# Kernel tuning notes

Measured on AMD Instinct MI355X. Metric: run time of the kernel, lower is better.

## Reference

```python
import jax, jax.numpy as jnp
import numpy as np

E = 1024      # embed_dim (== embed_dim_)
NH = 8        # num_heads
HD = E // NH  # head_dim
BS1 = 2048
BS2 = 2048
EPS = 1e-5


def _layernorm(x, g, b):
    m = jnp.mean(x, axis=-1, keepdims=True)
    v = jnp.mean(jnp.square(x - m), axis=-1, keepdims=True)
    return (x - m) * jax.lax.rsqrt(v + EPS) * g + b


def setup_inputs() -> dict:
    key = jax.random.key(0)
    ks = jax.random.split(key, 16)
    s = 1.0 / np.sqrt(E)
    s4 = 1.0 / np.sqrt(4 * E)
    inp = {
        "x1": jax.random.normal(ks[0], (BS1, E), jnp.float32),
        "x2": jax.random.normal(ks[1], (BS2, E), jnp.float32),
        "Wq": jax.random.uniform(ks[2], (E, E), jnp.float32, -s, s),
        "bq": jax.random.uniform(ks[3], (E,), jnp.float32, -s, s),
        "Wk": jax.random.uniform(ks[4], (E, E), jnp.float32, -s, s),
        "bk": jax.random.uniform(ks[5], (E,), jnp.float32, -s, s),
        "Wv": jax.random.uniform(ks[6], (E, E), jnp.float32, -s, s),
        "bv": jax.random.uniform(ks[7], (E,), jnp.float32, -s, s),
        "Wo": jax.random.uniform(ks[8], (E, E), jnp.float32, -s, s),
        "bo": jax.random.uniform(ks[9], (E,), jnp.float32, -s, s),
        "W1": jax.random.uniform(ks[10], (4 * E, E), jnp.float32, -s, s),
        "b1": jax.random.uniform(ks[11], (4 * E,), jnp.float32, -s, s),
        "W2": jax.random.uniform(ks[12], (E, 4 * E), jnp.float32, -s4, s4),
        "b2": jax.random.uniform(ks[13], (E,), jnp.float32, -s4, s4),
        "g1": jnp.ones((E,), jnp.float32),
        "be1": jnp.zeros((E,), jnp.float32),
        "g2": jnp.ones((E,), jnp.float32),
        "be2": jnp.zeros((E,), jnp.float32),
    }
    return inp


def reference(x1, x2, Wq, bq, Wk, bk, Wv, bv, Wo, bo, W1, b1, W2, b2, g1, be1, g2, be2):
    scale = HD ** -0.5
    # Projections; attention runs over the batch axis (n=bs1, m=bs2)
    q = (x1 @ Wq.T + bq).reshape(BS1, NH, HD)   # [n,h,d]
    k = (x2 @ Wk.T + bk).reshape(BS2, NH, HD)   # [m,h,d]
    v = (x2 @ Wv.T + bv).reshape(BS2, NH, HD)   # [m,h,d]
    scores = jnp.einsum('nhd,mhd->nmh', q, k) * scale  # [n,m,h]
    # NOTE: faithful to source: softmax over the HEADS axis (dim=-1)
    probs = jax.nn.softmax(scores, axis=-1)
    # dropout is identity in eval mode
    attn = jnp.einsum('nmh,mhd->nhd', probs, v).reshape(BS1, E)
    attn = attn @ Wo.T + bo
    h = _layernorm(x1 + attn, g1, be1)
    ffn = jax.nn.relu(h @ W1.T + b1) @ W2.T + b2
    return _layernorm(h + ffn, g2, be2)
```

## Files before the change

kernel.cpp:

```cpp
#include <hip/hip_runtime.h>

#define BS 2048
#define EMB 1024
#define NHEAD 8
#define HDIM 128

typedef unsigned short u16;
typedef __attribute__((ext_vector_type(8))) short bf16x8;
typedef __attribute__((ext_vector_type(4))) float f32x4;

__device__ __forceinline__ u16 f32_bf16(float f) {
  unsigned u = __float_as_uint(f);
  u += 0x7fffu + ((u >> 16) & 1u);
  return (u16)(u >> 16);
}
__device__ __forceinline__ float bf2f(u16 x) {
  return __uint_as_float((unsigned)x << 16);
}

__device__ __forceinline__ void gld_lds16(const void* g, void* l) {
  __builtin_amdgcn_global_load_lds(
      (const __attribute__((address_space(1))) void*)g,
      (__attribute__((address_space(3))) void*)l, 16, 0, 0);
}

struct CvtArgs { const float* src[8]; };
__global__ __launch_bounds__(256) void cvt_all(CvtArgs a, u16* __restrict__ dst) {
  long i = (long)blockIdx.x * 256 + threadIdx.x;
  int seg = (int)(i >> 18);
  const float* src; long b;
  if (seg < 2)       { src = a.src[0]; b = 0; }
  else if (seg < 4)  { src = a.src[1]; b = 2L << 18; }
  else if (seg == 4) { src = a.src[2]; b = 4L << 18; }
  else if (seg == 5) { src = a.src[3]; b = 5L << 18; }
  else if (seg == 6) { src = a.src[4]; b = 6L << 18; }
  else if (seg == 7) { src = a.src[5]; b = 7L << 18; }
  else if (seg < 12) { src = a.src[6]; b = 8L << 18; }
  else               { src = a.src[7]; b = 12L << 18; }
  float4 v = ((const float4*)src)[i - b];
  ushort4 o;
  o.x = f32_bf16(v.x); o.y = f32_bf16(v.y); o.z = f32_bf16(v.z); o.w = f32_bf16(v.w);
  ((ushort4*)dst)[i] = o;
}

__device__ __forceinline__ void gemm_core(
    const u16* __restrict__ A, const u16* __restrict__ B, void* __restrict__ Cp,
    const float* __restrict__ bias, int K, int lda, int ldb, int ldc,
    long cbase, int mode, int relu, int m0, int n0) {
  __shared__ __align__(16) u16 As[128 * 32];
  __shared__ __align__(16) u16 Bs[128 * 32];
  const int t = threadIdx.x;
  const int lane = t & 63, l15 = lane & 15, quad = lane >> 4;
  const int wv = t >> 6, wr = wv & 1, wc = wv >> 1;
  const int wbase = t & ~63;

  f32x4 acc[4][4];
#pragma unroll
  for (int r = 0; r < 4; ++r)
#pragma unroll
    for (int c = 0; c < 4; ++c) acc[r][c] = (f32x4){0.f, 0.f, 0.f, 0.f};

  for (int k0 = 0; k0 < K; k0 += 32) {
#pragma unroll
    for (int i = 0; i < 2; ++i) {
      int s = i * 256 + t;
      gld_lds16(A + (long)(m0 + (s >> 2)) * lda + k0 + (s & 3) * 8,
                As + (i * 256 + wbase) * 8);
    }
#pragma unroll
    for (int i = 0; i < 2; ++i) {
      int s = i * 256 + t;
      gld_lds16(B + (long)(n0 + (s >> 2)) * ldb + k0 + (s & 3) * 8,
                Bs + (i * 256 + wbase) * 8);
    }
    __syncthreads();
    bf16x8 fa[4], fb[4];
#pragma unroll
    for (int r = 0; r < 4; ++r)
      fa[r] = *(const bf16x8*)&As[(wr * 64 + r * 16 + l15) * 32 + quad * 8];
#pragma unroll
    for (int c = 0; c < 4; ++c)
      fb[c] = *(const bf16x8*)&Bs[(wc * 64 + c * 16 + l15) * 32 + quad * 8];
#pragma unroll
    for (int r = 0; r < 4; ++r)
#pragma unroll
      for (int c = 0; c < 4; ++c)
        acc[r][c] = __builtin_amdgcn_mfma_f32_16x16x32_bf16(fa[r], fb[c], acc[r][c], 0, 0, 0);
    __syncthreads();
  }

#pragma unroll
  for (int r = 0; r < 4; ++r)
#pragma unroll
    for (int c = 0; c < 4; ++c) {
      const int m = m0 + wr * 64 + r * 16 + quad * 4;
      const int n = n0 + wc * 64 + c * 16 + l15;
      const float bv = bias ? bias[n] : 0.f;
      f32x4 v = acc[r][c];
      if (mode == 2) {
        ushort4 o;
        o.x = f32_bf16(v[0] + bv);
        o.y = f32_bf16(v[1] + bv);
        o.z = f32_bf16(v[2] + bv);
        o.w = f32_bf16(v[3] + bv);
        *(ushort4*)((u16*)Cp + cbase + (long)n * ldc + m) = o;
      } else {
#pragma unroll
        for (int i = 0; i < 4; ++i) {
          float x = v[i] + bv;
          if (relu) x = fmaxf(x, 0.f);
          if (mode == 0)
            ((float*)Cp)[cbase + (long)(m + i) * ldc + n] = x;
          else
            ((u16*)Cp)[cbase + (long)(m + i) * ldc + n] = f32_bf16(x);
        }
      }
    }
}

__global__ __launch_bounds__(256) void gemm_bt_k(
    const u16* __restrict__ A, const u16* __restrict__ B, void* __restrict__ C,
    const float* __restrict__ bias, int K, int lda, int ldb, int ldc,
    long aOffZ, long bOffZ, long cOffZ, int mode, int relu) {
  gemm_core(A + (long)blockIdx.z * aOffZ, B + (long)blockIdx.z * bOffZ, C, bias,
            K, lda, ldb, ldc, (long)blockIdx.z * cOffZ, mode, relu,
            blockIdx.y * 128, blockIdx.x * 128);
}

__global__ __launch_bounds__(256) void qkv_kernel(
    const u16* __restrict__ x1b, const u16* __restrict__ x2b,
    const u16* __restrict__ Wqb, const u16* __restrict__ Wkb, const u16* __restrict__ Wvb,
    const float* __restrict__ bq, const float* __restrict__ bk, const float* __restrict__ bv,
    u16* __restrict__ Qb, u16* __restrict__ Kb, u16* __restrict__ Vt) {
  const int z = blockIdx.z;
  const u16* A = (z == 0) ? x1b : x2b;
  const u16* B = (z == 0) ? Wqb : (z == 1) ? Wkb : Wvb;
  void* C = (z == 0) ? (void*)Qb : (z == 1) ? (void*)Kb : (void*)Vt;
  const float* bias = (z == 0) ? bq : (z == 1) ? bk : bv;
  const int mode = (z == 2) ? 2 : 1;
  const int ldc = (z == 2) ? 2048 : 1024;
  gemm_core(A, B, C, bias, 1024, 1024, 1024, ldc, 0, mode, 0,
            blockIdx.y * 128, blockIdx.x * 128);
}

__global__ __launch_bounds__(1024, 4) void attn_fused(
    const u16* __restrict__ Q, const u16* __restrict__ Km, const u16* __restrict__ Vt,
    u16* __restrict__ p0, u16* __restrict__ p1, u16* __restrict__ p2, u16* __restrict__ p3) {
  __shared__ __align__(16) u16 KQ[2 * 20480];
  __shared__ __align__(16) u16 Ps[8 * 32 * 128];
  const int t = threadIdx.x;
  const int lane = t & 63, l15 = lane & 15, quad = lane >> 4;
  const int w = t >> 6;
  const int mw = w & 7, nh = w >> 3;
  const int n0 = blockIdx.x * 32;
  const int mz = blockIdx.y * 512;
  u16* part = (blockIdx.y == 0) ? p0 : (blockIdx.y == 1) ? p1 : (blockIdx.y == 2) ? p2 : p3;

  auto stage = [&](int snum, int bsel) {
    const int sh = (snum & 7) * 128;
    const int smb = mz + (snum >> 3) * 128;
#pragma unroll
    for (int i = 0; i < 3; ++i) {
      int G = i * 1024 + t;
      if (G < 2560) {
        int r = G >> 4, g = G & 15;
        const u16* src;
        if (i < 2) src = Km + (long)(smb + r) * 1024 + sh + ((g ^ (r & 7)) << 3);
        else       src = Q + (long)(n0 + r - 128) * 1024 + sh + ((g ^ (r & 7)) << 3);
        gld_lds16(src, KQ + bsel * 20480 + G * 8);
      }
    }
  };

  f32x4 accp[8];
#pragma unroll
  for (int c = 0; c < 8; ++c) accp[c] = (f32x4){0.f, 0.f, 0.f, 0.f};

  int b = 0;
  stage(0, 0);

  const int m = mw * 16 + l15;
  const int nq = nh * 16 + l15;
  const int sw3 = (l15 & 7) << 3;
  const int sw4 = (nq & 7) << 4;

  for (int it = 0; it < 4; ++it) {
    const int mb = mz + it * 128;
    f32x4 accs[8];
#pragma unroll
    for (int h = 0; h < 8; ++h) accs[h] = (f32x4){0.f, 0.f, 0.f, 0.f};

#pragma unroll
    for (int h = 0; h < 8; ++h) {
      __syncthreads();
      int ns = it * 8 + h + 1;
      if (ns < 32) stage(ns, b ^ 1);
      const u16* kb = KQ + b * 20480;
      const u16* qb = kb + 128 * 128;
#pragma unroll
      for (int kk = 0; kk < 4; ++kk) {
        int ko = (kk * 32 + quad * 8) ^ sw3;
        bf16x8 fa = *(const bf16x8*)&kb[m * 128 + ko];
        bf16x8 fb = *(const bf16x8*)&qb[nq * 128 + ko];
        accs[h] = __builtin_amdgcn_mfma_f32_16x16x32_bf16(fa, fb, accs[h], 0, 0, 0);
      }
      b ^= 1;
    }

    const float scale = 0.08838834764831845f;
#pragma unroll
    for (int i = 0; i < 4; ++i) {
      float mx = accs[0][i];
#pragma unroll
      for (int h = 1; h < 8; ++h) mx = fmaxf(mx, accs[h][i]);
      float sum = 0.f;
#pragma unroll
      for (int h = 0; h < 8; ++h) {
        float e = __expf((accs[h][i] - mx) * scale);
        accs[h][i] = e;
        sum += e;
      }
      float inv = 1.f / sum;
#pragma unroll
      for (int h = 0; h < 8; ++h) accs[h][i] *= inv;
    }
#pragma unroll
    for (int h = 0; h < 8; ++h) {
      ushort4 o;
      o.x = f32_bf16(accs[h][0]);
      o.y = f32_bf16(accs[h][1]);
      o.z = f32_bf16(accs[h][2]);
      o.w = f32_bf16(accs[h][3]);
      *(ushort4*)((char*)Ps + h * 8192 + nq * 256 + ((mw * 32 + quad * 8) ^ sw4)) = o;
    }
    __syncthreads();
#pragma unroll
    for (int mq = 0; mq < 4; ++mq) {
      bf16x8 vf[8];
#pragma unroll
      for (int c = 0; c < 8; ++c)
        vf[c] = *(const bf16x8*)&Vt[(long)(mw * 128 + c * 16 + l15) * 2048 +
                                    mb + mq * 32 + quad * 8];
      bf16x8 pa = *(const bf16x8*)((const char*)Ps + mw * 8192 + nq * 256 +
                                   ((mq * 64 + quad * 16) ^ sw4));
#pragma unroll
      for (int c = 0; c < 8; ++c)
        accp[c] = __builtin_amdgcn_mfma_f32_16x16x32_bf16(pa, vf[c], accp[c], 0, 0, 0);
    }
  }
#pragma unroll
  for (int c = 0; c < 8; ++c)
#pragma unroll
    for (int i = 0; i < 4; ++i)
      part[(long)(n0 + nh * 16 + quad * 4 + i) * 1024 + mw * 128 + c * 16 + l15] =
          f32_bf16(accp[c][i]);
}

__global__ __launch_bounds__(256) void reduce4p_bf16(
    const u16* __restrict__ p0, const u16* __restrict__ p1,
    const u16* __restrict__ p2, const u16* __restrict__ p3, u16* __restrict__ out) {
  long i = (long)blockIdx.x * 256 + threadIdx.x;
  ushort4 a = ((const ushort4*)p0)[i];
  ushort4 b = ((const ushort4*)p1)[i];
  ushort4 c = ((const ushort4*)p2)[i];
  ushort4 d = ((const ushort4*)p3)[i];
  ushort4 o;
  o.x = f32_bf16(bf2f(a.x) + bf2f(b.x) + bf2f(c.x) + bf2f(d.x));
  o.y = f32_bf16(bf2f(a.y) + bf2f(b.y) + bf2f(c.y) + bf2f(d.y));
  o.z = f32_bf16(bf2f(a.z) + bf2f(b.z) + bf2f(c.z) + bf2f(d.z));
  o.w = f32_bf16(bf2f(a.w) + bf2f(b.w) + bf2f(c.w) + bf2f(d.w));
  ((ushort4*)out)[i] = o;
}

__global__ __launch_bounds__(256) void ln_residual_p4(
    const float* __restrict__ x,
    const u16* __restrict__ p0, const u16* __restrict__ p1,
    const u16* __restrict__ p2, const u16* __restrict__ p3,
    const float* __restrict__ colb, const float* __restrict__ g, const float* __restrict__ b,
    float* __restrict__ out32, u16* __restrict__ out16) {
  const int row = blockIdx.x, t = threadIdx.x;
  const long base = (long)row * EMB;
  float4 v = ((const float4*)(x + base))[t];
  ushort4 a0 = ((const ushort4*)(p0 + base))[t];
  ushort4 a1 = ((const ushort4*)(p1 + base))[t];
  ushort4 a2 = ((const ushort4*)(p2 + base))[t];
  ushort4 a3 = ((const ushort4*)(p3 + base))[t];
  float4 cb = ((const float4*)colb)[t];
  v.x += bf2f(a0.x) + bf2f(a1.x) + bf2f(a2.x) + bf2f(a3.x) + cb.x;
  v.y += bf2f(a0.y) + bf2f(a1.y) + bf2f(a2.y) + bf2f(a3.y) + cb.y;
  v.z += bf2f(a0.z) + bf2f(a1.z) + bf2f(a2.z) + bf2f(a3.z) + cb.z;
  v.w += bf2f(a0.w) + bf2f(a1.w) + bf2f(a2.w) + bf2f(a3.w) + cb.w;
  float s = v.x + v.y + v.z + v.w;
  float q = v.x * v.x + v.y * v.y + v.z * v.z + v.w * v.w;
#pragma unroll
  for (int off = 32; off > 0; off >>= 1) {
    s += __shfl_xor(s, off);
    q += __shfl_xor(q, off);
  }
  __shared__ float red[8];
  const int wv = t >> 6, lane = t & 63;
  if (lane == 0) { red[wv] = s; red[4 + wv] = q; }
  __syncthreads();
  s = red[0] + red[1] + red[2] + red[3];
  q = red[4] + red[5] + red[6] + red[7];
  const float mean = s * (1.f / EMB);
  const float var = q * (1.f / EMB) - mean * mean;
  const float rstd = rsqrtf(var + 1e-5f);
  float4 gg = ((const float4*)g)[t];
  float4 bb = ((const float4*)b)[t];
  float4 o;
  o.x = (v.x - mean) * rstd * gg.x + bb.x;
  o.y = (v.y - mean) * rstd * gg.y + bb.y;
  o.z = (v.z - mean) * rstd * gg.z + bb.z;
  o.w = (v.w - mean) * rstd * gg.w + bb.w;
  ((float4*)(out32 + base))[t] = o;
  if (out16) {
    ushort4 ho;
    ho.x = f32_bf16(o.x); ho.y = f32_bf16(o.y); ho.z = f32_bf16(o.z); ho.w = f32_bf16(o.w);
    ((ushort4*)(out16 + base))[t] = ho;
  }
}

extern "C" void kernel_launch(void* const* d_in, const int* in_sizes, int n_in,
                              void* d_out, int out_size, void* d_ws, size_t ws_size,
                              hipStream_t stream) {
  const float* x1 = (const float*)d_in[0];
  const float* x2 = (const float*)d_in[1];
  const float* Wq = (const float*)d_in[2];
  const float* bq = (const float*)d_in[3];
  const float* Wk = (const float*)d_in[4];
  const float* bk = (const float*)d_in[5];
  const float* Wv = (const float*)d_in[6];
  const float* bv = (const float*)d_in[7];
  const float* Wo = (const float*)d_in[8];
  const float* bo = (const float*)d_in[9];
  const float* W1 = (const float*)d_in[10];
  const float* b1 = (const float*)d_in[11];
  const float* W2 = (const float*)d_in[12];
  const float* b2 = (const float*)d_in[13];
  const float* g1 = (const float*)d_in[14];
  const float* be1 = (const float*)d_in[15];
  const float* g2 = (const float*)d_in[16];
  const float* be2 = (const float*)d_in[17];

  char* ws = (char*)d_ws;
  const size_t MB = 1ull << 20;
  u16* x1b = (u16*)(ws + 0 * MB);
  u16* x2b = (u16*)(ws + 4 * MB);
  u16* Wqb = (u16*)(ws + 8 * MB);
  u16* Wkb = (u16*)(ws + 10 * MB);
  u16* Wvb = (u16*)(ws + 12 * MB);
  u16* Wob = (u16*)(ws + 14 * MB);
  u16* W1b = (u16*)(ws + 16 * MB);
  u16* W2b = (u16*)(ws + 24 * MB);
  u16* Qb  = (u16*)(ws + 32 * MB);
  u16* Kb  = (u16*)(ws + 36 * MB);
  u16* Vtb = (u16*)(ws + 40 * MB);
  u16* attnb = (u16*)(ws + 44 * MB);
  u16* aP[4] = {(u16*)(ws + 48 * MB), (u16*)(ws + 52 * MB),
                (u16*)(ws + 56 * MB), (u16*)(ws + 60 * MB)};
  u16* woP[4] = {(u16*)(ws + 48 * MB), (u16*)(ws + 52 * MB),
                 (u16*)(ws + 56 * MB), (u16*)(ws + 60 * MB)};
  float* h32  = (float*)(ws + 64 * MB);
  u16*  h16   = (u16*)(ws + 72 * MB);
  u16*  ffn1b = (u16*)(ws + 76 * MB);
  u16* f2P[4] = {(u16*)(ws + 92 * MB), (u16*)(ws + 96 * MB),
                 (u16*)(ws + 100 * MB), (u16*)(ws + 104 * MB)};

  CvtArgs ca;
  ca.src[0] = x1; ca.src[1] = x2; ca.src[2] = Wq; ca.src[3] = Wk;
  ca.src[4] = Wv; ca.src[5] = Wo; ca.src[6] = W1; ca.src[7] = W2;
  cvt_all<<<16384, 256, 0, stream>>>(ca, (u16*)ws);

  qkv_kernel<<<dim3(8, 16, 3), 256, 0, stream>>>(x1b, x2b, Wqb, Wkb, Wvb, bq, bk, bv, Qb, Kb, Vtb);

  attn_fused<<<dim3(64, 4), 1024, 0, stream>>>(Qb, Kb, Vtb, aP[0], aP[1], aP[2], aP[3]);

  reduce4p_bf16<<<2048, 256, 0, stream>>>(aP[0], aP[1], aP[2], aP[3], attnb);

  gemm_bt_k<<<dim3(8, 16, 4), 256, 0, stream>>>(attnb, Wob, woP[0], nullptr,
                                                256, 1024, 1024, 1024,
                                                256, 256, (long)BS * 1024, 1, 0);

  ln_residual_p4<<<2048, 256, 0, stream>>>(x1, woP[0], woP[1], woP[2], woP[3],
                                           bo, g1, be1, h32, h16);

  gemm_bt_k<<<dim3(32, 16, 1), 256, 0, stream>>>(h16, W1b, ffn1b, b1,
                                                 1024, 1024, 1024, 4096,
                                                 0, 0, 0, 1, 1);

  gemm_bt_k<<<dim3(8, 16, 4), 256, 0, stream>>>(ffn1b, W2b, f2P[0], nullptr,
                                                1024, 4096, 4096, 1024,
                                                1024, 1024, (long)BS * 1024, 1, 0);

  ln_residual_p4<<<2048, 256, 0, stream>>>(h32, f2P[0], f2P[1], f2P[2], f2P[3],
                                           b2, g2, be2, (float*)d_out, nullptr);
}
```

Before: 370.0 us.

## Split attention key axis eight ways with 512-thread blocks and 8-way reduce

The fused attention kernel now uses 512-thread blocks that each cover 256 keys instead of 512. This doubles the grid to 512 blocks, and each warp now handles one head across both 16-row query groups in the P·V phase. The shared staging buffers and the probability tile are shrunk to match. The partial outputs become one contiguous array of eight slices, summed by a new 8-way reduction kernel. The aim is better CU occupancy and less serialization per block, at the cost of twice the partial-sum write and read traffic.

```diff
diff --git a/kernel.cpp b/kernel.cpp
--- a/kernel.cpp
+++ b/kernel.cpp
@@ -143,38 +143,38 @@
             blockIdx.y * 128, blockIdx.x * 128);
 }
 
-__global__ __launch_bounds__(1024, 4) void attn_fused(
+__global__ __launch_bounds__(512, 4) void attn_fused(
     const u16* __restrict__ Q, const u16* __restrict__ Km, const u16* __restrict__ Vt,
-    u16* __restrict__ p0, u16* __restrict__ p1, u16* __restrict__ p2, u16* __restrict__ p3) {
-  __shared__ __align__(16) u16 KQ[2 * 20480];
-  __shared__ __align__(16) u16 Ps[8 * 32 * 128];
+    u16* __restrict__ aP) {
+  __shared__ __align__(16) u16 KQ[2 * 12288];
+  __shared__ __align__(16) u16 Ps[8 * 32 * 64];
   const int t = threadIdx.x;
   const int lane = t & 63, l15 = lane & 15, quad = lane >> 4;
   const int w = t >> 6;
-  const int mw = w & 7, nh = w >> 3;
+  const int mw = w & 3, nh = w >> 2;
   const int n0 = blockIdx.x * 32;
-  const int mz = blockIdx.y * 512;
-  u16* part = (blockIdx.y == 0) ? p0 : (blockIdx.y == 1) ? p1 : (blockIdx.y == 2) ? p2 : p3;
+  const int mz = blockIdx.y * 256;
+  u16* part = aP + (long)blockIdx.y * BS * 1024;
 
   auto stage = [&](int snum, int bsel) {
     const int sh = (snum & 7) * 128;
-    const int smb = mz + (snum >> 3) * 128;
+    const int smb = mz + (snum >> 3) * 64;
 #pragma unroll
     for (int i = 0; i < 3; ++i) {
-      int G = i * 1024 + t;
-      if (G < 2560) {
-        int r = G >> 4, g = G & 15;
-        const u16* src;
-        if (i < 2) src = Km + (long)(smb + r) * 1024 + sh + ((g ^ (r & 7)) << 3);
-        else       src = Q + (long)(n0 + r - 128) * 1024 + sh + ((g ^ (r & 7)) << 3);
-        gld_lds16(src, KQ + bsel * 20480 + G * 8);
-      }
+      int G = i * 512 + t;
+      int r = G >> 4, g = G & 15;
+      const u16* src;
+      if (i < 2) src = Km + (long)(smb + r) * 1024 + sh + ((g ^ (r & 7)) << 3);
+      else       src = Q + (long)(n0 + r - 64) * 1024 + sh + ((g ^ (r & 7)) << 3);
+      gld_lds16(src, KQ + bsel * 12288 + G * 8);
     }
   };
 
-  f32x4 accp[8];
-#pragma unroll
-  for (int c = 0; c < 8; ++c) accp[c] = (f32x4){0.f, 0.f, 0.f, 0.f};
+  f32x4 accp[2][8];
+#pragma unroll
+  for (int r = 0; r < 2; ++r)
+#pragma unroll
+    for (int c = 0; c < 8; ++c) accp[r][c] = (f32x4){0.f, 0.f, 0.f, 0.f};
 
   int b = 0;
   stage(0, 0);
@@ -182,10 +182,10 @@
   const int m = mw * 16 + l15;
   const int nq = nh * 16 + l15;
   const int sw3 = (l15 & 7) << 3;
-  const int sw4 = (nq & 7) << 4;
+  const int sw4 = (l15 & 7) << 4;
 
   for (int it = 0; it < 4; ++it) {
-    const int mb = mz + it * 128;
+    const int mb = mz + it * 64;
     f32x4 accs[8];
 #pragma unroll
     for (int h = 0; h < 8; ++h) accs[h] = (f32x4){0.f, 0.f, 0.f, 0.f};
@@ -195,8 +195,8 @@
       __syncthreads();
       int ns = it * 8 + h + 1;
       if (ns < 32) stage(ns, b ^ 1);
-      const u16* kb = KQ + b * 20480;
-      const u16* qb = kb + 128 * 128;
+      const u16* kb = KQ + b * 12288;
+      const u16* qb = kb + 64 * 128;
 #pragma unroll
       for (int kk = 0; kk < 4; ++kk) {
         int ko = (kk * 32 + quad * 8) ^ sw3;
@@ -231,44 +231,50 @@
       o.y = f32_bf16(accs[h][1]);
       o.z = f32_bf16(accs[h][2]);
       o.w = f32_bf16(accs[h][3]);
-      *(ushort4*)((char*)Ps + h * 8192 + nq * 256 + ((mw * 32 + quad * 8) ^ sw4)) = o;
+      *(ushort4*)((char*)Ps + h * 4096 + nq * 128 + ((mw * 32 + quad * 8) ^ sw4)) = o;
     }
     __syncthreads();
 #pragma unroll
-    for (int mq = 0; mq < 4; ++mq) {
+    for (int mq = 0; mq < 2; ++mq) {
       bf16x8 vf[8];
 #pragma unroll
       for (int c = 0; c < 8; ++c)
-        vf[c] = *(const bf16x8*)&Vt[(long)(mw * 128 + c * 16 + l15) * 2048 +
+        vf[c] = *(const bf16x8*)&Vt[(long)(w * 128 + c * 16 + l15) * 2048 +
                                     mb + mq * 32 + quad * 8];
-      bf16x8 pa = *(const bf16x8*)((const char*)Ps + mw * 8192 + nq * 256 +
-                                   ((mq * 64 + quad * 16) ^ sw4));
+      bf16x8 pa[2];
+#pragma unroll
+      for (int r = 0; r < 2; ++r)
+        pa[r] = *(const bf16x8*)((const char*)Ps + w * 4096 + (r * 16 + l15) * 128 +
+                                 ((mq * 64 + quad * 16) ^ sw4));
 #pragma unroll
       for (int c = 0; c < 8; ++c)
-        accp[c] = __builtin_amdgcn_mfma_f32_16x16x32_bf16(pa, vf[c], accp[c], 0, 0, 0);
+#pragma unroll
+        for (int r = 0; r < 2; ++r)
+          accp[r][c] = __builtin_amdgcn_mfma_f32_16x16x32_bf16(pa[r], vf[c], accp[r][c], 0, 0, 0);
     }
   }
 #pragma unroll
-  for (int c = 0; c < 8; ++c)
-#pragma unroll
-    for (int i = 0; i < 4; ++i)
-      part[(long)(n0 + nh * 16 + quad * 4 + i) * 1024 + mw * 128 + c * 16 + l15] =
-          f32_bf16(accp[c][i]);
-}
-
-__global__ __launch_bounds__(256) void reduce4p_bf16(
-    const u16* __restrict__ p0, const u16* __restrict__ p1,
-    const u16* __restrict__ p2, const u16* __restrict__ p3, u16* __restrict__ out) {
+  for (int r = 0; r < 2; ++r)
+#pragma unroll
+    for (int c = 0; c < 8; ++c)
+#pragma unroll
+      for (int i = 0; i < 4; ++i)
+        part[(long)(n0 + r * 16 + quad * 4 + i) * 1024 + w * 128 + c * 16 + l15] =
+            f32_bf16(accp[r][c][i]);
+}
+
+__global__ __launch_bounds__(256) void reduce8p_bf16(
+    const u16* __restrict__ base, u16* __restrict__ out) {
   long i = (long)blockIdx.x * 256 + threadIdx.x;
-  ushort4 a = ((const ushort4*)p0)[i];
-  ushort4 b = ((const ushort4*)p1)[i];
-  ushort4 c = ((const ushort4*)p2)[i];
-  ushort4 d = ((const ushort4*)p3)[i];
+  const long stride = (long)BS * 1024 / 4;
+  float sx = 0.f, sy = 0.f, sz = 0.f, sw = 0.f;
+#pragma unroll
+  for (int k = 0; k < 8; ++k) {
+    ushort4 a = ((const ushort4*)base)[i + k * stride];
+    sx += bf2f(a.x); sy += bf2f(a.y); sz += bf2f(a.z); sw += bf2f(a.w);
+  }
   ushort4 o;
-  o.x = f32_bf16(bf2f(a.x) + bf2f(b.x) + bf2f(c.x) + bf2f(d.x));
-  o.y = f32_bf16(bf2f(a.y) + bf2f(b.y) + bf2f(c.y) + bf2f(d.y));
-  o.z = f32_bf16(bf2f(a.z) + bf2f(b.z) + bf2f(c.z) + bf2f(d.z));
-  o.w = f32_bf16(bf2f(a.w) + bf2f(b.w) + bf2f(c.w) + bf2f(d.w));
+  o.x = f32_bf16(sx); o.y = f32_bf16(sy); o.z = f32_bf16(sz); o.w = f32_bf16(sw);
   ((ushort4*)out)[i] = o;
 }
 
@@ -357,8 +363,7 @@
   u16* Kb  = (u16*)(ws + 36 * MB);
   u16* Vtb = (u16*)(ws + 40 * MB);
   u16* attnb = (u16*)(ws + 44 * MB);
-  u16* aP[4] = {(u16*)(ws + 48 * MB), (u16*)(ws + 52 * MB),
-                (u16*)(ws + 56 * MB), (u16*)(ws + 60 * MB)};
+  u16* aP = (u16*)(ws + 48 * MB);
   u16* woP[4] = {(u16*)(ws + 48 * MB), (u16*)(ws + 52 * MB),
                  (u16*)(ws + 56 * MB), (u16*)(ws + 60 * MB)};
   float* h32  = (float*)(ws + 64 * MB);
@@ -374,9 +379,9 @@
 
   qkv_kernel<<<dim3(8, 16, 3), 256, 0, stream>>>(x1b, x2b, Wqb, Wkb, Wvb, bq, bk, bv, Qb, Kb, Vtb);
 
-  attn_fused<<<dim3(64, 4), 1024, 0, stream>>>(Qb, Kb, Vtb, aP[0], aP[1], aP[2], aP[3]);
-
-  reduce4p_bf16<<<2048, 256, 0, stream>>>(aP[0], aP[1], aP[2], aP[3], attnb);
+  attn_fused<<<dim3(64, 8), 512, 0, stream>>>(Qb, Kb, Vtb, aP);
+
+  reduce8p_bf16<<<2048, 256, 0, stream>>>(aP, attnb);
 
   gemm_bt_k<<<dim3(8, 16, 4), 256, 0, stream>>>(attnb, Wob, woP[0], nullptr,
                                                 256, 1024, 1024, 1024,
```

New measurement: 357.8 us. -3.3%, faster.
